# Optimization experiments

Measured on AMD Instinct MI355X. Metric: run time of the kernel, lower is better.

The kernel has to match this reference:

```python
import jax, jax.numpy as jnp
import numpy as np

WS = 32          # window_size; N = WS*WS tokens
NH = 8           # num_heads
HD = 64          # head_dim
DIM = 512        # model dim (= NH*HD)
B = 16
N = WS * WS


def _rel_index() -> np.ndarray:
    """Relative position index, identical to the torch __init__ construction."""
    coords = np.stack(np.meshgrid(np.arange(WS), np.arange(WS), indexing='ij'))
    coords = coords.reshape(2, -1)                       # [2, N]
    rel = coords[:, :, None] - coords[:, None, :]        # [2, N, N]
    rel = rel.transpose(1, 2, 0).copy()                  # [N, N, 2]
    rel[..., 0] += WS - 1
    rel[..., 1] += WS - 1
    rel[..., 0] *= 2 * WS - 1
    return rel.sum(-1).astype(np.int32)                  # [N, N], values in [0, (2WS-1)^2)


def setup_inputs() -> dict:
    key = jax.random.key(0)
    ks = jax.random.split(key, 5)
    s = DIM ** -0.5
    return {
        "x": jax.random.normal(ks[0], (B, N, DIM), jnp.float32),
        "qkv_w": jax.random.normal(ks[1], (3 * NH * HD, DIM), jnp.float32) * s,
        "qkv_b": jnp.zeros((3 * NH * HD,), jnp.float32),
        "proj_w": jax.random.normal(ks[2], (DIM, NH * HD), jnp.float32) * s,
        "proj_b": jnp.zeros((DIM,), jnp.float32),
        "bias_table": jax.random.normal(ks[3], ((2 * WS - 1) ** 2, NH), jnp.float32) * 0.02,
        "rel_index": jnp.asarray(_rel_index()),
    }


def reference(x, qkv_w, qkv_b, proj_w, proj_b, bias_table, rel_index):
    Bb, Nn, C = x.shape
    qkv = (x @ qkv_w.T + qkv_b).reshape(Bb, Nn, 3, NH, HD)
    q, k, v = jnp.moveaxis(qkv, 2, 0)                    # each [B, N, NH, HD]
    q = q * (HD ** -0.5)
    attn = jnp.einsum('bnhd,bmhd->bhnm', q, k)           # [B, NH, N, N]
    bias = bias_table[rel_index]                         # gather -> [N, N, NH]
    attn = attn + jnp.transpose(bias, (2, 0, 1))[None]
    attn = jax.nn.softmax(attn, axis=-1)                 # dropout p=0 (eval)
    out = jnp.einsum('bhnm,bmhd->bnhd', attn, v).reshape(Bb, Nn, NH * HD)
    out = out @ proj_w.T + proj_b                        # [B, N, DIM]
    return jnp.transpose(out, (0, 2, 1)).reshape(Bb, DIM, WS, WS)
```

## Files before the change

### kernel.cpp

```cpp
#include <hip/hip_runtime.h>
#include <hip/hip_bf16.h>


typedef __attribute__((ext_vector_type(4))) float  f32x4;
typedef __attribute__((ext_vector_type(8))) short  s16x8;
typedef __attribute__((ext_vector_type(4))) short  s16x4;

#define LOG2E 1.44269504f

__device__ __forceinline__ short f2bf(float f) {
    union { float f; unsigned u; } v; v.f = f;
    unsigned r = v.u + 0x7fffu + ((v.u >> 16) & 1u);
    return (short)(r >> 16);
}
__device__ __forceinline__ float u2f(unsigned u) {
    union { unsigned u; float f; } v; v.u = u; return v.f;
}
__device__ __forceinline__ unsigned cvtpk(float lo, float hi) {
    unsigned r;
    asm("v_cvt_pk_bf16_f32 %0, %1, %2" : "=v"(r) : "v"(lo), "v"(hi));
    return r;
}
__device__ __forceinline__ s16x8 ld_frag(const short* p) {
    s16x4 lo = *(const s16x4*)p;
    s16x4 hi = *(const s16x4*)(p + 4);
    s16x8 v;
    v[0]=lo[0]; v[1]=lo[1]; v[2]=lo[2]; v[3]=lo[3];
    v[4]=hi[0]; v[5]=hi[1]; v[6]=hi[2]; v[7]=hi[3];
    return v;
}
__device__ __forceinline__ void st8(short* p, s16x8 v) {
    s16x4 lo, hi;
    lo[0]=v[0]; lo[1]=v[1]; lo[2]=v[2]; lo[3]=v[3];
    hi[0]=v[4]; hi[1]=v[5]; hi[2]=v[6]; hi[3]=v[7];
    *(s16x4*)p = lo;
    *(s16x4*)(p + 4) = hi;
}
__device__ __forceinline__ void gl_lds16(const short* g, short* l) {
    __builtin_amdgcn_global_load_lds(
        (const __attribute__((address_space(1))) unsigned int*)g,
        (__attribute__((address_space(3))) unsigned int*)l,
        16, 0, 0);
}

__global__ __launch_bounds__(256) void prep_kernel(
    const float* __restrict__ x, const float* __restrict__ qkv_w,
    const float* __restrict__ proj_w,
    const float* __restrict__ table, const int* __restrict__ ridx,
    short* __restrict__ xb, short* __restrict__ wqkv, short* __restrict__ wproj,
    short* __restrict__ bx)
{
    int bid = blockIdx.x, tid = threadIdx.x;
    if (bid < 9216) {
        const float* src; short* dst; int i;
        if (bid < 8192)      { src = x;      dst = xb;    i = bid * 256 + tid; }
        else if (bid < 8960) { src = qkv_w;  dst = wqkv;  i = (bid - 8192) * 256 + tid; }
        else                 { src = proj_w; dst = wproj; i = (bid - 8960) * 256 + tid; }
        f32x4 v = ((const f32x4*)src)[i];
        s16x4 o;
        o[0]=f2bf(v[0]); o[1]=f2bf(v[1]); o[2]=f2bf(v[2]); o[3]=f2bf(v[3]);
        ((s16x4*)dst)[i] = o;
    } else {
        int i = (bid - 9216) * 256 + tid;
        int n = i >> 10, m = i & 1023;
        int idx = ridx[i];
        const float* t = table + idx * 8;
        int pos = ((n*8 + (m >> 7))*4 + ((m >> 2) & 3))*32 + ((m >> 4) & 7)*4 + (m & 3);
        #pragma unroll
        for (int h = 0; h < 8; h++)
            bx[h * 1048576 + pos] = f2bf(t[h] * LOG2E);
    }
}

__global__ __launch_bounds__(256) void qkv_gemm(
    const short* __restrict__ Xb, const short* __restrict__ W,
    const float* __restrict__ bias,
    short* __restrict__ qb, short* __restrict__ kb, short* __restrict__ vtb)
{
    __shared__ __align__(16) short smem[16384];
    short* As = smem;
    short* Bs = smem + 8192;
    const int tid = threadIdx.x;
    const int lane = tid & 63, w = tid >> 6;
    const int quad = lane >> 4, l16 = lane & 15;
    const int m0 = blockIdx.x * 128, n0 = blockIdx.y * 128;
    const int wm = (w >> 1) * 64, wn = (w & 1) * 64;
    f32x4 acc[4][4] = {};

    const int ri = lane >> 3;
    const int u  = lane & 7;
    const bool trq = (n0 < 1024);

    for (int k0 = 0; k0 < 512; k0 += 64) {
        __syncthreads();
        #pragma unroll
        for (int q = 0; q < 4; q++) {
            int rb = w*32 + q*8;
            int r  = rb + ri;
            int cu = u ^ ri;
            gl_lds16(Xb + (m0 + r)*512 + k0 + cu*8, As + rb*64);
            gl_lds16(W  + (n0 + r)*512 + k0 + cu*8, Bs + rb*64);
        }
        __syncthreads();
        #pragma unroll
        for (int hf = 0; hf < 2; hf++) {
            s16x8 af[4], bfr[4];
            #pragma unroll
            for (int i = 0; i < 4; i++) {
                int row = wm + i*16 + l16;
                af[i] = *(const s16x8*)(As + row*64 + ((hf*4 + quad) ^ (row & 7))*8);
            }
            #pragma unroll
            for (int j = 0; j < 4; j++) {
                int row = wn + j*16 + l16;
                bfr[j] = *(const s16x8*)(Bs + row*64 + ((hf*4 + quad) ^ (row & 7))*8);
            }
            if (trq) {
                #pragma unroll
                for (int i = 0; i < 4; i++)
                    #pragma unroll
                    for (int j = 0; j < 4; j++)
                        acc[i][j] = __builtin_amdgcn_mfma_f32_16x16x32_bf16(bfr[j], af[i], acc[i][j], 0, 0, 0);
            } else {
                #pragma unroll
                for (int i = 0; i < 4; i++)
                    #pragma unroll
                    for (int j = 0; j < 4; j++)
                        acc[i][j] = __builtin_amdgcn_mfma_f32_16x16x32_bf16(af[i], bfr[j], acc[i][j], 0, 0, 0);
            }
        }
    }

    if (trq) {
        #pragma unroll
        for (int j = 0; j < 4; j++) {
            int c0 = n0 + wn + j*16 + quad*4;
            int which = c0 >> 9, hh = (c0 & 511) >> 6, d0 = c0 & 63;
            f32x4 bv = *(const f32x4*)&bias[c0];
            #pragma unroll
            for (int i = 0; i < 4; i++) {
                int row = m0 + wm + i*16 + l16;
                int bi = row >> 10, n = row & 1023;
                float v0 = acc[i][j][0] + bv[0], v1 = acc[i][j][1] + bv[1];
                float v2 = acc[i][j][2] + bv[2], v3 = acc[i][j][3] + bv[3];
                uint2 pk;
                if (which == 0) {
                    const float sc = 0.125f * LOG2E;
                    pk.x = cvtpk(v0*sc, v1*sc); pk.y = cvtpk(v2*sc, v3*sc);
                    *(uint2*)&qb[((bi*8 + hh)*1024 + n)*64 + d0] = pk;
                } else {
                    pk.x = cvtpk(v0, v1); pk.y = cvtpk(v2, v3);
                    *(uint2*)&kb[((bi*8 + hh)*1024 + n)*64 + d0] = pk;
                }
            }
        }
    } else {
        #pragma unroll
        for (int j = 0; j < 4; j++) {
            int col = n0 + wn + j*16 + l16;
            int rem = col & 511, hh = rem >> 6, d = rem & 63;
            float bv = bias[col];
            #pragma unroll
            for (int i = 0; i < 4; i++) {
                int row = m0 + wm + i*16 + quad*4;
                int bi = row >> 10, n = row & 1023;
                float v0 = acc[i][j][0] + bv, v1 = acc[i][j][1] + bv;
                float v2 = acc[i][j][2] + bv, v3 = acc[i][j][3] + bv;
                uint2 pk; pk.x = cvtpk(v0, v1); pk.y = cvtpk(v2, v3);
                *(uint2*)&vtb[((bi*8 + hh)*64 + d)*1024 + n] = pk;
            }
        }
    }
}

__global__ __launch_bounds__(512, 4) void attn_kernel(
    const short* __restrict__ qbuf, const short* __restrict__ kbuf,
    const short* __restrict__ vtbuf, const short* __restrict__ bxp,
    short* __restrict__ ao)
{
    __shared__ __align__(16) short smem[25344];
    short* R1 = smem;
    short* Vs = smem + 16896;

    const int bh = blockIdx.x;
    const int b = bh >> 3, h = bh & 7;
    const int q0 = blockIdx.y * 128;
    const int tid = threadIdx.x, lane = tid & 63, w = tid >> 6;
    const int quad = lane >> 4, l16 = lane & 15;

    const short* qg = qbuf + (bh*1024 + q0) * 64;
    const short* kg = kbuf + bh * 65536;
    const short* vg = vtbuf + bh * 65536;

    {
        int r = tid >> 3, c = (tid & 7) * 8;
        #pragma unroll
        for (int p = 0; p < 2; p++)
            st8(&R1[(r + p*64)*68 + c], *(const s16x8*)(qg + (r + p*64)*64 + c));
    }
    __syncthreads();
    s16x8 aq[2];
    aq[0] = ld_frag(&R1[(w*16 + l16)*68 + quad*8]);
    aq[1] = ld_frag(&R1[(w*16 + l16)*68 + 32 + quad*8]);

    float lrow = 0.f;
    f32x4 oacc[4] = {};
    short* Pw = R1 + w * 2112;
    const short* bbase = bxp + h*1048576 + ((q0 + w*16 + l16)*8)*128 + quad*32;

    for (int it = 0; it < 8; it++) {
        const int k0 = it * 128;
        __syncthreads();

        uint4 bw[4];
        {
            const uint4* bp = (const uint4*)(bbase + it*128);
            #pragma unroll
            for (int j = 0; j < 4; j++) bw[j] = bp[j];
        }

        {
            int r = tid >> 3, c = (tid & 7) * 8;
            #pragma unroll
            for (int p = 0; p < 2; p++)
                st8(&R1[(r + p*64)*68 + c], *(const s16x8*)(kg + (k0 + r + p*64)*64 + c));
        }
        {
            int r = tid >> 4, c = (tid & 15) * 8;
            #pragma unroll
            for (int p = 0; p < 2; p++)
                st8(&Vs[(r + p*32)*132 + c], *(const s16x8*)(vg + (r + p*32)*1024 + k0 + c));
        }
        __syncthreads();

        f32x4 s[8];
        __builtin_amdgcn_s_setprio(1);
        #pragma unroll
        for (int nf = 0; nf < 8; nf++) {
            unsigned ua = (nf & 1) ? bw[nf >> 1].z : bw[nf >> 1].x;
            unsigned ub = (nf & 1) ? bw[nf >> 1].w : bw[nf >> 1].y;
            s[nf][0] = u2f(ua << 16); s[nf][1] = u2f(ua & 0xffff0000u);
            s[nf][2] = u2f(ub << 16); s[nf][3] = u2f(ub & 0xffff0000u);
            s16x8 bk0 = ld_frag(&R1[(nf*16 + l16)*68 + quad*8]);
            s16x8 bk1 = ld_frag(&R1[(nf*16 + l16)*68 + 32 + quad*8]);
            s[nf] = __builtin_amdgcn_mfma_f32_16x16x32_bf16(bk0, aq[0], s[nf], 0, 0, 0);
            s[nf] = __builtin_amdgcn_mfma_f32_16x16x32_bf16(bk1, aq[1], s[nf], 0, 0, 0);
        }
        __builtin_amdgcn_s_setprio(0);

        float rs = 0.f;
        #pragma unroll
        for (int nf = 0; nf < 8; nf++)
            #pragma unroll
            for (int r = 0; r < 4; r++) {
                float p = __builtin_exp2f(s[nf][r]);
                s[nf][r] = p;
                rs += p;
            }
        lrow += rs;

        __syncthreads();

        #pragma unroll
        for (int nf = 0; nf < 8; nf++) {
            uint2 pk;
            pk.x = cvtpk(s[nf][0], s[nf][1]);
            pk.y = cvtpk(s[nf][2], s[nf][3]);
            *(uint2*)&Pw[l16*132 + nf*16 + quad*4] = pk;
        }
        asm volatile("s_waitcnt lgkmcnt(0)" ::: "memory");

        __builtin_amdgcn_s_setprio(1);
        #pragma unroll
        for (int ks = 0; ks < 4; ks++) {
            s16x8 ap = ld_frag(&Pw[l16*132 + ks*32 + quad*8]);
            #pragma unroll
            for (int df = 0; df < 4; df++) {
                s16x8 bv = ld_frag(&Vs[(df*16 + l16)*132 + ks*32 + quad*8]);
                oacc[df] = __builtin_amdgcn_mfma_f32_16x16x32_bf16(ap, bv, oacc[df], 0, 0, 0);
            }
        }
        __builtin_amdgcn_s_setprio(0);
    }

    lrow += __shfl_xor(lrow, 16);
    lrow += __shfl_xor(lrow, 32);
    float inv_r[4];
    #pragma unroll
    for (int r = 0; r < 4; r++) inv_r[r] = 1.0f / __shfl(lrow, quad*4 + r);
    #pragma unroll
    for (int r = 0; r < 4; r++) {
        int n = q0 + w*16 + quad*4 + r;
        #pragma unroll
        for (int df = 0; df < 4; df++)
            ao[(b*1024 + n)*512 + h*64 + df*16 + l16] = f2bf(oacc[df][r] * inv_r[r]);
    }
}

__global__ __launch_bounds__(256) void proj_gemm(
    const short* __restrict__ A, const short* __restrict__ W,
    const float* __restrict__ bias, float* __restrict__ out)
{
    __shared__ __align__(16) short smemp[16384];
    short* As = smemp;
    short* Bs = smemp + 8192;
    const int tid = threadIdx.x;
    const int lane = tid & 63, w = tid >> 6;
    const int quad = lane >> 4, l16 = lane & 15;
    const int m0 = blockIdx.x * 128, n0 = blockIdx.y * 128;
    const int wm = (w >> 1) * 64, wn = (w & 1) * 64;
    f32x4 acc[4][4] = {};

    const int ri = lane >> 3;
    const int u  = lane & 7;

    for (int k0 = 0; k0 < 512; k0 += 64) {
        __syncthreads();
        #pragma unroll
        for (int q = 0; q < 4; q++) {
            int rb = w*32 + q*8;
            int r  = rb + ri;
            int cu = u ^ ri;
            gl_lds16(A + (m0 + r)*512 + k0 + cu*8, As + rb*64);
            gl_lds16(W + (n0 + r)*512 + k0 + cu*8, Bs + rb*64);
        }
        __syncthreads();
        #pragma unroll
        for (int hf = 0; hf < 2; hf++) {
            s16x8 af[4], bfr[4];
            #pragma unroll
            for (int i = 0; i < 4; i++) {
                int row = wm + i*16 + l16;
                af[i] = *(const s16x8*)(As + row*64 + ((hf*4 + quad) ^ (row & 7))*8);
            }
            #pragma unroll
            for (int j = 0; j < 4; j++) {
                int row = wn + j*16 + l16;
                bfr[j] = *(const s16x8*)(Bs + row*64 + ((hf*4 + quad) ^ (row & 7))*8);
            }
            #pragma unroll
            for (int i = 0; i < 4; i++)
                #pragma unroll
                for (int j = 0; j < 4; j++)
                    acc[i][j] = __builtin_amdgcn_mfma_f32_16x16x32_bf16(af[i], bfr[j], acc[i][j], 0, 0, 0);
        }
    }

    const int bi = m0 >> 10, nbase = m0 & 1023;
    #pragma unroll
    for (int j = 0; j < 4; j++) {
        int c = n0 + wn + j*16 + l16;
        float bv = bias[c];
        #pragma unroll
        for (int i = 0; i < 4; i++) {
            f32x4 v = acc[i][j];
            v[0] += bv; v[1] += bv; v[2] += bv; v[3] += bv;
            *(f32x4*)&out[(bi*512 + c)*1024 + nbase + wm + i*16 + quad*4] = v;
        }
    }
}

extern "C" void kernel_launch(void* const* d_in, const int* in_sizes, int n_in,
                              void* d_out, int out_size, void* d_ws, size_t ws_size,
                              hipStream_t stream) {
    const float* x      = (const float*)d_in[0];
    const float* qkv_w  = (const float*)d_in[1];
    const float* qkv_b  = (const float*)d_in[2];
    const float* proj_w = (const float*)d_in[3];
    const float* proj_b = (const float*)d_in[4];
    const float* btab   = (const float*)d_in[5];
    const int*   ridx   = (const int*)d_in[6];
    float* out = (float*)d_out;

    short* ws    = (short*)d_ws;
    short* wqkv  = ws;
    short* wproj = wqkv + 1536*512;
    short* qb    = wproj + 512*512;
    short* kb    = qb  + 16*8*1024*64;
    short* vtb   = kb  + 16*8*1024*64;
    short* bx    = vtb + 16*8*1024*64;
    short* ao    = bx  + 8*1024*1024;
    short* xb    = ao;

    prep_kernel<<<13312, 256, 0, stream>>>(x, qkv_w, proj_w, btab, ridx, xb, wqkv, wproj, bx);
    qkv_gemm<<<dim3(128, 12), 256, 0, stream>>>(xb, wqkv, qkv_b, qb, kb, vtb);
    attn_kernel<<<dim3(128, 8), 512, 0, stream>>>(qb, kb, vtb, bx, ao);
    proj_gemm<<<dim3(128, 4), 256, 0, stream>>>(ao, wproj, proj_b, out);
}
```

Measured before the change: 230.9 us.

## Double-buffer GEMM K-tiles and compute softmax row sums via MFMA

The QKV and projection GEMMs switch from single-buffered 64-wide K tiles to double-buffered 32-wide K tiles. The next tile's global-to-LDS load is issued before computing on the current one, so there is one barrier per half-step instead of two per step. The attention kernel drops the scalar exp-sum accumulation and the cross-lane shuffles. Instead it computes the row sums with an extra MFMA of P against a ones vector. The sum now uses the bf16-rounded probabilities, and st8 picks up a redundant duplicated assignment.

New measurement: 236.1 us. +2.2%, slower.

```diff
diff --git a/kernel.cpp b/kernel.cpp
--- a/kernel.cpp
+++ b/kernel.cpp
@@ -32,7 +32,8 @@
 __device__ __forceinline__ void st8(short* p, s16x8 v) {
     s16x4 lo, hi;
     lo[0]=v[0]; lo[1]=v[1]; lo[2]=v[2]; lo[3]=v[3];
-    hi[0]=v[4]; hi[1]=v[5]; hi[2]=v[6]; hi[3]=v[7];
+    hi[0]=v[4]; hi[1]=v[5]; hi[2]=v[6]; hi[7-4]=v[7];
+    hi[2]=v[6]; hi[3]=v[7];
     *(s16x4*)p = lo;
     *(s16x4*)(p + 4) = hi;
 }
@@ -78,8 +79,8 @@
     short* __restrict__ qb, short* __restrict__ kb, short* __restrict__ vtb)
 {
     __shared__ __align__(16) short smem[16384];
-    short* As = smem;
-    short* Bs = smem + 8192;
+    short* As0 = smem;           short* As1 = smem + 4096;
+    short* Bs0 = smem + 8192;    short* Bs1 = smem + 12288;
     const int tid = threadIdx.x;
     const int lane = tid & 63, w = tid >> 6;
     const int quad = lane >> 4, l16 = lane & 15;
@@ -87,48 +88,57 @@
     const int wm = (w >> 1) * 64, wn = (w & 1) * 64;
     f32x4 acc[4][4] = {};
 
-    const int ri = lane >> 3;
-    const int u  = lane & 7;
+    const int ri = lane >> 2;
+    const int u  = lane & 3;
     const bool trq = (n0 < 1024);
 
+    auto STAGE = [&](int k0, short* Adst, short* Bdst) {
+        #pragma unroll
+        for (int p = 0; p < 2; p++) {
+            int rb = w*32 + p*16;
+            int r  = rb + ri;
+            int cu = u ^ ((r >> 1) & 3);
+            gl_lds16(Xb + (m0 + r)*512 + k0 + cu*8, Adst + rb*32);
+            gl_lds16(W  + (n0 + r)*512 + k0 + cu*8, Bdst + rb*32);
+        }
+    };
+    auto COMPUTE = [&](const short* Asrc, const short* Bsrc) {
+        s16x8 af[4], bfr[4];
+        #pragma unroll
+        for (int i = 0; i < 4; i++) {
+            int row = wm + i*16 + l16;
+            af[i] = *(const s16x8*)(Asrc + row*32 + (quad ^ ((row >> 1) & 3))*8);
+        }
+        #pragma unroll
+        for (int j = 0; j < 4; j++) {
+            int row = wn + j*16 + l16;
+            bfr[j] = *(const s16x8*)(Bsrc + row*32 + (quad ^ ((row >> 1) & 3))*8);
+        }
+        if (trq) {
+            #pragma unroll
+            for (int i = 0; i < 4; i++)
+                #pragma unroll
+                for (int j = 0; j < 4; j++)
+                    acc[i][j] = __builtin_amdgcn_mfma_f32_16x16x32_bf16(bfr[j], af[i], acc[i][j], 0, 0, 0);
+        } else {
+            #pragma unroll
+            for (int i = 0; i < 4; i++)
+                #pragma unroll
+                for (int j = 0; j < 4; j++)
+                    acc[i][j] = __builtin_amdgcn_mfma_f32_16x16x32_bf16(af[i], bfr[j], acc[i][j], 0, 0, 0);
+        }
+    };
+
+    STAGE(0, As0, Bs0);
+    __syncthreads();
+    #pragma unroll
     for (int k0 = 0; k0 < 512; k0 += 64) {
-        __syncthreads();
-        #pragma unroll
-        for (int q = 0; q < 4; q++) {
-            int rb = w*32 + q*8;
-            int r  = rb + ri;
-            int cu = u ^ ri;
-            gl_lds16(Xb + (m0 + r)*512 + k0 + cu*8, As + rb*64);
-            gl_lds16(W  + (n0 + r)*512 + k0 + cu*8, Bs + rb*64);
-        }
-        __syncthreads();
-        #pragma unroll
-        for (int hf = 0; hf < 2; hf++) {
-            s16x8 af[4], bfr[4];
-            #pragma unroll
-            for (int i = 0; i < 4; i++) {
-                int row = wm + i*16 + l16;
-                af[i] = *(const s16x8*)(As + row*64 + ((hf*4 + quad) ^ (row & 7))*8);
-            }
-            #pragma unroll
-            for (int j = 0; j < 4; j++) {
-                int row = wn + j*16 + l16;
-                bfr[j] = *(const s16x8*)(Bs + row*64 + ((hf*4 + quad) ^ (row & 7))*8);
-            }
-            if (trq) {
-                #pragma unroll
-                for (int i = 0; i < 4; i++)
-                    #pragma unroll
-                    for (int j = 0; j < 4; j++)
-                        acc[i][j] = __builtin_amdgcn_mfma_f32_16x16x32_bf16(bfr[j], af[i], acc[i][j], 0, 0, 0);
-            } else {
-                #pragma unroll
-                for (int i = 0; i < 4; i++)
-                    #pragma unroll
-                    for (int j = 0; j < 4; j++)
-                        acc[i][j] = __builtin_amdgcn_mfma_f32_16x16x32_bf16(af[i], bfr[j], acc[i][j], 0, 0, 0);
-            }
-        }
+        if (k0 + 32 < 512) STAGE(k0 + 32, As1, Bs1);
+        COMPUTE(As0, Bs0);
+        __syncthreads();
+        if (k0 + 64 < 512) STAGE(k0 + 64, As0, Bs0);
+        COMPUTE(As1, Bs1);
+        __syncthreads();
     }
 
     if (trq) {
@@ -203,8 +213,13 @@
     aq[0] = ld_frag(&R1[(w*16 + l16)*68 + quad*8]);
     aq[1] = ld_frag(&R1[(w*16 + l16)*68 + 32 + quad*8]);
 
-    float lrow = 0.f;
     f32x4 oacc[4] = {};
+    f32x4 sacc = {};
+    const short one_bf = (short)0x3F80;
+    s16x8 vones;
+    vones[0]=one_bf; vones[1]=one_bf; vones[2]=one_bf; vones[3]=one_bf;
+    vones[4]=one_bf; vones[5]=one_bf; vones[6]=one_bf; vones[7]=one_bf;
+
     short* Pw = R1 + w * 2112;
     const short* bbase = bxp + h*1048576 + ((q0 + w*16 + l16)*8)*128 + quad*32;
 
@@ -248,16 +263,11 @@
         }
         __builtin_amdgcn_s_setprio(0);
 
-        float rs = 0.f;
         #pragma unroll
         for (int nf = 0; nf < 8; nf++)
             #pragma unroll
-            for (int r = 0; r < 4; r++) {
-                float p = __builtin_exp2f(s[nf][r]);
-                s[nf][r] = p;
-                rs += p;
-            }
-        lrow += rs;
+            for (int r = 0; r < 4; r++)
+                s[nf][r] = __builtin_exp2f(s[nf][r]);
 
         __syncthreads();
 
@@ -279,15 +289,14 @@
                 s16x8 bv = ld_frag(&Vs[(df*16 + l16)*132 + ks*32 + quad*8]);
                 oacc[df] = __builtin_amdgcn_mfma_f32_16x16x32_bf16(ap, bv, oacc[df], 0, 0, 0);
             }
+            sacc = __builtin_amdgcn_mfma_f32_16x16x32_bf16(ap, vones, sacc, 0, 0, 0);
         }
         __builtin_amdgcn_s_setprio(0);
     }
 
-    lrow += __shfl_xor(lrow, 16);
-    lrow += __shfl_xor(lrow, 32);
     float inv_r[4];
     #pragma unroll
-    for (int r = 0; r < 4; r++) inv_r[r] = 1.0f / __shfl(lrow, quad*4 + r);
+    for (int r = 0; r < 4; r++) inv_r[r] = 1.0f / sacc[r];
     #pragma unroll
     for (int r = 0; r < 4; r++) {
         int n = q0 + w*16 + quad*4 + r;
@@ -302,8 +311,8 @@
     const float* __restrict__ bias, float* __restrict__ out)
 {
     __shared__ __align__(16) short smemp[16384];
-    short* As = smemp;
-    short* Bs = smemp + 8192;
+    short* As0 = smemp;          short* As1 = smemp + 4096;
+    short* Bs0 = smemp + 8192;   short* Bs1 = smemp + 12288;
     const int tid = threadIdx.x;
     const int lane = tid & 63, w = tid >> 6;
     const int quad = lane >> 4, l16 = lane & 15;
@@ -311,39 +320,48 @@
     const int wm = (w >> 1) * 64, wn = (w & 1) * 64;
     f32x4 acc[4][4] = {};
 
-    const int ri = lane >> 3;
-    const int u  = lane & 7;
-
+    const int ri = lane >> 2;
+    const int u  = lane & 3;
+
+    auto STAGE = [&](int k0, short* Adst, short* Bdst) {
+        #pragma unroll
+        for (int p = 0; p < 2; p++) {
+            int rb = w*32 + p*16;
+            int r  = rb + ri;
+            int cu = u ^ ((r >> 1) & 3);
+            gl_lds16(A + (m0 + r)*512 + k0 + cu*8, Adst + rb*32);
+            gl_lds16(W + (n0 + r)*512 + k0 + cu*8, Bdst + rb*32);
+        }
+    };
+    auto COMPUTE = [&](const short* Asrc, const short* Bsrc) {
+        s16x8 af[4], bfr[4];
+        #pragma unroll
+        for (int i = 0; i < 4; i++) {
+            int row = wm + i*16 + l16;
+            af[i] = *(const s16x8*)(Asrc + row*32 + (quad ^ ((row >> 1) & 3))*8);
+        }
+        #pragma unroll
+        for (int j = 0; j < 4; j++) {
+            int row = wn + j*16 + l16;
+            bfr[j] = *(const s16x8*)(Bsrc + row*32 + (quad ^ ((row >> 1) & 3))*8);
+        }
+        #pragma unroll
+        for (int i = 0; i < 4; i++)
+            #pragma unroll
+            for (int j = 0; j < 4; j++)
+                acc[i][j] = __builtin_amdgcn_mfma_f32_16x16x32_bf16(af[i], bfr[j], acc[i][j], 0, 0, 0);
+    };
+
+    STAGE(0, As0, Bs0);
+    __syncthreads();
+    #pragma unroll
     for (int k0 = 0; k0 < 512; k0 += 64) {
-        __syncthreads();
-        #pragma unroll
-        for (int q = 0; q < 4; q++) {
-            int rb = w*32 + q*8;
-            int r  = rb + ri;
-            int cu = u ^ ri;
-            gl_lds16(A + (m0 + r)*512 + k0 + cu*8, As + rb*64);
-            gl_lds16(W + (n0 + r)*512 + k0 + cu*8, Bs + rb*64);
-        }
-        __syncthreads();
-        #pragma unroll
-        for (int hf = 0; hf < 2; hf++) {
-            s16x8 af[4], bfr[4];
-            #pragma unroll
-            for (int i = 0; i < 4; i++) {
-                int row = wm + i*16 + l16;
-                af[i] = *(const s16x8*)(As + row*64 + ((hf*4 + quad) ^ (row & 7))*8);
-            }
-            #pragma unroll
-            for (int j = 0; j < 4; j++) {
-                int row = wn + j*16 + l16;
-                bfr[j] = *(const s16x8*)(Bs + row*64 + ((hf*4 + quad) ^ (row & 7))*8);
-            }
-            #pragma unroll
-            for (int i = 0; i < 4; i++)
-                #pragma unroll
-                for (int j = 0; j < 4; j++)
-                    acc[i][j] = __builtin_amdgcn_mfma_f32_16x16x32_bf16(af[i], bfr[j], acc[i][j], 0, 0, 0);
-        }
+        if (k0 + 32 < 512) STAGE(k0 + 32, As1, Bs1);
+        COMPUTE(As0, Bs0);
+        __syncthreads();
+        if (k0 + 64 < 512) STAGE(k0 + 64, As0, Bs0);
+        COMPUTE(As1, Bs1);
+        __syncthreads();
     }
 
     const int bi = m0 >> 10, nbase = m0 & 1023;
```
